# Kernel optimization log

Measured on AMD Instinct MI355X. Metric: run time of the kernel, lower is better.

## Reference

```python
import jax, jax.numpy as jnp
import numpy as np

B, T, D = 32, 1024, 768
H = 768          # GRU hidden size
INNER = 512      # fc output size
NOUT = 39        # out_proj outputs (13 classes x 3 ACCDOA coords)


def setup_inputs() -> dict:
    key = jax.random.key(0)
    ks = jax.random.split(key, 16)
    s_in = 1.0 / np.sqrt(H)
    inp = {
        "features": jax.random.normal(ks[0], (B, T, D), jnp.float32),
        "padding_mask": jnp.zeros((B, T), jnp.bool_),
        # GRU layer 0 (input D -> H), PyTorch gate order [r, z, n]
        "w_ih0": jax.random.uniform(ks[1], (3 * H, D), jnp.float32, -s_in, s_in),
        "w_hh0": jax.random.uniform(ks[2], (3 * H, H), jnp.float32, -s_in, s_in),
        "b_ih0": jax.random.uniform(ks[3], (3 * H,), jnp.float32, -s_in, s_in),
        "b_hh0": jax.random.uniform(ks[4], (3 * H,), jnp.float32, -s_in, s_in),
        # GRU layer 1 (H -> H)
        "w_ih1": jax.random.uniform(ks[5], (3 * H, H), jnp.float32, -s_in, s_in),
        "w_hh1": jax.random.uniform(ks[6], (3 * H, H), jnp.float32, -s_in, s_in),
        "b_ih1": jax.random.uniform(ks[7], (3 * H,), jnp.float32, -s_in, s_in),
        "b_hh1": jax.random.uniform(ks[8], (3 * H,), jnp.float32, -s_in, s_in),
        # fc: hidden -> inner, then SELU
        "fc_w": jax.random.uniform(ks[9], (INNER, H), jnp.float32, -s_in, s_in),
        "fc_b": jax.random.uniform(ks[10], (INNER,), jnp.float32, -s_in, s_in),
        # out_proj: inner -> num_outs, then tanh
        "out_w": jax.random.uniform(ks[11], (NOUT, INNER), jnp.float32, -1.0 / np.sqrt(INNER), 1.0 / np.sqrt(INNER)),
        "out_b": jax.random.uniform(ks[12], (NOUT,), jnp.float32, -1.0 / np.sqrt(INNER), 1.0 / np.sqrt(INNER)),
    }
    return inp


def _gru_layer(x, w_ih, w_hh, b_ih, b_hh):
    # x: [B, T, Din] -> [B, T, H]; PyTorch GRU math, gate order r,z,n
    b, t, _ = x.shape
    h = w_hh.shape[1]
    # precompute input projections for all timesteps in one big GEMM
    x_proj = jnp.einsum('btd,gd->btg', x, w_ih) + b_ih  # [B, T, 3H]

    def step(h_prev, xp):
        gi_r, gi_z, gi_n = jnp.split(xp, 3, axis=-1)
        gh = h_prev @ w_hh.T + b_hh
        gh_r, gh_z, gh_n = jnp.split(gh, 3, axis=-1)
        r = jax.nn.sigmoid(gi_r + gh_r)
        z = jax.nn.sigmoid(gi_z + gh_z)
        n = jnp.tanh(gi_n + r * gh_n)
        h_new = (1.0 - z) * n + z * h_prev
        return h_new, h_new

    h0 = jnp.zeros((b, h), x.dtype)
    _, ys = jax.lax.scan(step, h0, jnp.swapaxes(x_proj, 0, 1))  # ys: [T, B, H]
    return jnp.swapaxes(ys, 0, 1)


def reference(features, padding_mask, w_ih0, w_hh0, b_ih0, b_hh0,
              w_ih1, w_hh1, b_ih1, b_hh1, fc_w, fc_b, out_w, out_b):
    # dropout_input p=0.0 -> identity (eval); padding_mask unused by forward math
    x = _gru_layer(features, w_ih0, w_hh0, b_ih0, b_hh0)
    x = _gru_layer(x, w_ih1, w_hh1, b_ih1, b_hh1)
    x = jax.nn.selu(x @ fc_w.T + fc_b)          # fc + activation_fn='selu'
    x = jnp.tanh(x @ out_w.T + out_b)           # out_proj + out_activation 'tanh'
    return x
```

## Files before the change

### kernel.cpp

```cpp
#include <hip/hip_runtime.h>
#include <cstdint>

typedef float vf2 __attribute__((ext_vector_type(2)));

#define GB_M 128
#define GB_N 64
#define GB_K 16

__global__ __launch_bounds__(256) void gemm_bt_f32(
    const float* __restrict__ A, const float* __restrict__ B,
    const float* __restrict__ bias, float* __restrict__ C,
    int Mc, int N, int K, int tc_shift, int Tfull, int t0, int act)
{
  __shared__ float As[GB_K][GB_M + 4];
  __shared__ float Bs[GB_K][GB_N + 4];
  const int tid = threadIdx.x;
  const int m0 = blockIdx.y * GB_M;
  const int n0 = blockIdx.x * GB_N;
  const int tx = tid & 15;
  const int ty = tid >> 4;

  const int tcmask = (1 << tc_shift) - 1;
  int arow[2];
#pragma unroll
  for (int i = 0; i < 2; i++) {
    int f = tid + i * 256;
    int row = f >> 2;
    int rc = m0 + row;
    arow[i] = (rc >> tc_shift) * Tfull + t0 + (rc & tcmask);
  }
  const int akq = tid & 3;
  const int brow = tid >> 2;
  const int bn = n0 + brow;

  vf2 acc2[4][4];
#pragma unroll
  for (int i = 0; i < 4; i++)
#pragma unroll
    for (int j = 0; j < 4; j++) acc2[i][j] = (vf2)(0.f);

  for (int k0 = 0; k0 < K; k0 += GB_K) {
#pragma unroll
    for (int i = 0; i < 2; i++) {
      int f = tid + i * 256;
      int row = f >> 2;
      float4 v = *(const float4*)(A + (size_t)arow[i] * K + k0 + akq * 4);
      As[akq * 4 + 0][row] = v.x; As[akq * 4 + 1][row] = v.y;
      As[akq * 4 + 2][row] = v.z; As[akq * 4 + 3][row] = v.w;
    }
    {
      float4 v = make_float4(0.f, 0.f, 0.f, 0.f);
      if (bn < N) v = *(const float4*)(B + (size_t)bn * K + k0 + akq * 4);
      Bs[akq * 4 + 0][brow] = v.x; Bs[akq * 4 + 1][brow] = v.y;
      Bs[akq * 4 + 2][brow] = v.z; Bs[akq * 4 + 3][brow] = v.w;
    }
    __syncthreads();
#pragma unroll
    for (int k = 0; k < GB_K; k++) {
      float4 a0 = *(const float4*)&As[k][ty * 8];
      float4 a1 = *(const float4*)&As[k][ty * 8 + 4];
      float4 b0 = *(const float4*)&Bs[k][tx * 4];
      vf2 a2[4];
      a2[0] = (vf2){a0.x, a0.y}; a2[1] = (vf2){a0.z, a0.w};
      a2[2] = (vf2){a1.x, a1.y}; a2[3] = (vf2){a1.z, a1.w};
      float bv[4] = {b0.x, b0.y, b0.z, b0.w};
#pragma unroll
      for (int j = 0; j < 4; j++) {
        vf2 bs = (vf2){bv[j], bv[j]};
#pragma unroll
        for (int ip = 0; ip < 4; ip++)
          acc2[ip][j] = __builtin_elementwise_fma(a2[ip], bs, acc2[ip][j]);
      }
    }
    __syncthreads();
  }

#pragma unroll
  for (int j = 0; j < 4; j++) {
    int n = n0 + tx * 4 + j;
    if (n >= N) continue;
    float bz = bias[n];
#pragma unroll
    for (int i = 0; i < 8; i++) {
      int m = m0 + ty * 8 + i;
      float x = ((i & 1) ? acc2[i >> 1][j].y : acc2[i >> 1][j].x) + bz;
      if (act == 1) {
        x = 1.0507009873554805f * (x > 0.f ? x : 1.6732632423543772f * (__expf(x) - 1.f));
      } else if (act == 2) {
        x = tanhf(x);
      }
      C[(size_t)m * N + n] = x;
    }
  }
}

#define RT 384
#define RNWG 256

__global__ __launch_bounds__(RT, 1) void gru_rec(
    const float* __restrict__ gi, const float* __restrict__ w_hh,
    const float* __restrict__ b_hh, unsigned long long* __restrict__ gx,
    float* __restrict__ seq, int t0, int Tc)
{
  __shared__ float hs[8][776];
  const int wg = blockIdx.x;
  const int jg = wg & 63;
  const int sd = wg >> 6;
  const int j0 = jg * 12;
  const int tid = threadIdx.x;
  const int p  = tid >> 6;
  const int ks = tid & 63;

  float4 wreg[3][2][3];
#pragma unroll
  for (int g = 0; g < 3; g++)
#pragma unroll
    for (int j2 = 0; j2 < 2; j2++)
#pragma unroll
      for (int kk = 0; kk < 3; kk++)
        wreg[g][j2][kk] = *(const float4*)(
            w_hh + (size_t)(g * 768 + j0 + 2 * p + j2) * 768 + (kk * 64 + ks) * 4);

  const int j2l = (ks >> 2) & 1;
  const int cl  = ks & 3;
  const int j_out  = j0 + 2 * p + j2l;
  const int bX_out = 8 * sd + cl;
  const int bY_out = 8 * sd + 4 + cl;
  const float bhr = b_hh[j_out];
  const float bhz = b_hh[768 + j_out];
  const float bhn = b_hh[1536 + j_out];

  const int sbi = tid >> 6;
  const int sk  = tid & 63;

  const bool hi4 = (ks & 4) != 0;
  const bool hi2 = (ks & 2) != 0;
  const bool hi1 = (ks & 1) != 0;

  for (int tt = 0; tt < Tc; tt++) {
    const int t = t0 + tt;
    const unsigned wantt = (unsigned)t;

    float gXr = 0.f, gXz = 0.f, gXn = 0.f;
    if (ks < 8) {
      const float* gX = gi + ((size_t)bX_out * Tc + tt) * 2304 + j_out;
      gXr = gX[0]; gXz = gX[768]; gXn = gX[1536];
    }
    if (tid < 256) {
      const unsigned long long* src =
          gx + (size_t)(t & 1) * 24576 + (size_t)(8 * sd + sbi) * 768 + sk;
      unsigned long long v[12];
#pragma unroll
      for (int i = 0; i < 12; i++)
        v[i] = __hip_atomic_load(src + 64 * i, __ATOMIC_RELAXED, __HIP_MEMORY_SCOPE_AGENT);
      while (true) {
        unsigned miss = 0;
#pragma unroll
        for (int i = 0; i < 12; i++)
          miss |= (unsigned)((unsigned)(v[i] >> 32) < wantt);
        if (!miss) break;
        __builtin_amdgcn_s_sleep(1);
#pragma unroll
        for (int i = 0; i < 12; i++)
          if ((unsigned)(v[i] >> 32) < wantt)
            v[i] = __hip_atomic_load(src + 64 * i, __ATOMIC_RELAXED, __HIP_MEMORY_SCOPE_AGENT);
      }
#pragma unroll
      for (int i = 0; i < 12; i++)
        hs[sbi][sk + 64 * i] = __uint_as_float((unsigned)v[i]);
    }
    __syncthreads();

    float r3[3];
    {
      vf2 a2[3][2][4];
#pragma unroll
      for (int g = 0; g < 3; g++)
#pragma unroll
        for (int j2 = 0; j2 < 2; j2++)
#pragma unroll
          for (int c = 0; c < 4; c++) a2[g][j2][c] = (vf2)(0.f);
#pragma unroll
      for (int kk = 0; kk < 3; kk++) {
        const int off = (kk * 64 + ks) * 4;
        vf2 hlo[4], hhi[4];
#pragma unroll
        for (int c = 0; c < 4; c++) {
          float4 h = *(const float4*)(&hs[c][0] + off);
          hlo[c] = (vf2){h.x, h.y};
          hhi[c] = (vf2){h.z, h.w};
        }
#pragma unroll
        for (int g = 0; g < 3; g++)
#pragma unroll
          for (int j2 = 0; j2 < 2; j2++) {
            float4 w = wreg[g][j2][kk];
            vf2 wlo = (vf2){w.x, w.y};
            vf2 whi = (vf2){w.z, w.w};
#pragma unroll
            for (int c = 0; c < 4; c++) {
              a2[g][j2][c] = __builtin_elementwise_fma(wlo, hlo[c], a2[g][j2][c]);
              a2[g][j2][c] = __builtin_elementwise_fma(whi, hhi[c], a2[g][j2][c]);
            }
          }
      }
      float acc[3][2][4];
#pragma unroll
      for (int g = 0; g < 3; g++)
#pragma unroll
        for (int j2 = 0; j2 < 2; j2++)
#pragma unroll
          for (int c = 0; c < 4; c++) acc[g][j2][c] = a2[g][j2][c].x + a2[g][j2][c].y;

      float r12[3][4];
#pragma unroll
      for (int g = 0; g < 3; g++)
#pragma unroll
        for (int c = 0; c < 4; c++) {
          float send = hi4 ? acc[g][0][c] : acc[g][1][c];
          float keep = hi4 ? acc[g][1][c] : acc[g][0][c];
          r12[g][c] = keep + __shfl_xor(send, 4);
        }
      float r6[3][2];
#pragma unroll
      for (int g = 0; g < 3; g++)
#pragma unroll
        for (int c2 = 0; c2 < 2; c2++) {
          float send = hi2 ? r12[g][c2] : r12[g][2 + c2];
          float keep = hi2 ? r12[g][2 + c2] : r12[g][c2];
          r6[g][c2] = keep + __shfl_xor(send, 2);
        }
#pragma unroll
      for (int g = 0; g < 3; g++) {
        float send = hi1 ? r6[g][0] : r6[g][1];
        float keep = hi1 ? r6[g][1] : r6[g][0];
        r3[g] = keep + __shfl_xor(send, 1);
      }
#pragma unroll
      for (int g = 0; g < 3; g++) {
        r3[g] += __shfl_xor(r3[g], 8);
        r3[g] += __shfl_xor(r3[g], 16);
        r3[g] += __shfl_xor(r3[g], 32);
      }
    }
    if (ks < 8) {
      float hp = hs[cl][j_out];
      float r = 1.f / (1.f + __expf(-(gXr + r3[0] + bhr)));
      float z = 1.f / (1.f + __expf(-(gXz + r3[1] + bhz)));
      float n = tanhf(gXn + r * (r3[2] + bhn));
      float hv = (1.f - z) * n + z * hp;
      __hip_atomic_store(
          gx + (size_t)((t + 1) & 1) * 24576 + (size_t)bX_out * 768 + j_out,
          ((unsigned long long)(unsigned)(t + 1) << 32) |
              (unsigned long long)__float_as_uint(hv),
          __ATOMIC_RELAXED, __HIP_MEMORY_SCOPE_AGENT);
      seq[((size_t)bX_out * 1024 + t) * 768 + j_out] = hv;
    }

    float gYr = 0.f, gYz = 0.f, gYn = 0.f;
    if (ks < 8) {
      const float* gY = gi + ((size_t)bY_out * Tc + tt) * 2304 + j_out;
      gYr = gY[0]; gYz = gY[768]; gYn = gY[1536];
    }
    if (tid < 256) {
      const unsigned long long* src =
          gx + (size_t)(t & 1) * 24576 + (size_t)(8 * sd + 4 + sbi) * 768 + sk;
      unsigned long long v[12];
#pragma unroll
      for (int i = 0; i < 12; i++)
        v[i] = __hip_atomic_load(src + 64 * i, __ATOMIC_RELAXED, __HIP_MEMORY_SCOPE_AGENT);
      while (true) {
        unsigned miss = 0;
#pragma unroll
        for (int i = 0; i < 12; i++)
          miss |= (unsigned)((unsigned)(v[i] >> 32) < wantt);
        if (!miss) break;
        __builtin_amdgcn_s_sleep(1);
#pragma unroll
        for (int i = 0; i < 12; i++)
          if ((unsigned)(v[i] >> 32) < wantt)
            v[i] = __hip_atomic_load(src + 64 * i, __ATOMIC_RELAXED, __HIP_MEMORY_SCOPE_AGENT);
      }
#pragma unroll
      for (int i = 0; i < 12; i++)
        hs[4 + sbi][sk + 64 * i] = __uint_as_float((unsigned)v[i]);
    }
    __syncthreads();

    {
      vf2 a2[3][2][4];
#pragma unroll
      for (int g = 0; g < 3; g++)
#pragma unroll
        for (int j2 = 0; j2 < 2; j2++)
#pragma unroll
          for (int c = 0; c < 4; c++) a2[g][j2][c] = (vf2)(0.f);
#pragma unroll
      for (int kk = 0; kk < 3; kk++) {
        const int off = (kk * 64 + ks) * 4;
        vf2 hlo[4], hhi[4];
#pragma unroll
        for (int c = 0; c < 4; c++) {
          float4 h = *(const float4*)(&hs[4 + c][0] + off);
          hlo[c] = (vf2){h.x, h.y};
          hhi[c] = (vf2){h.z, h.w};
        }
#pragma unroll
        for (int g = 0; g < 3; g++)
#pragma unroll
          for (int j2 = 0; j2 < 2; j2++) {
            float4 w = wreg[g][j2][kk];
            vf2 wlo = (vf2){w.x, w.y};
            vf2 whi = (vf2){w.z, w.w};
#pragma unroll
            for (int c = 0; c < 4; c++) {
              a2[g][j2][c] = __builtin_elementwise_fma(wlo, hlo[c], a2[g][j2][c]);
              a2[g][j2][c] = __builtin_elementwise_fma(whi, hhi[c], a2[g][j2][c]);
            }
          }
      }
      float acc[3][2][4];
#pragma unroll
      for (int g = 0; g < 3; g++)
#pragma unroll
        for (int j2 = 0; j2 < 2; j2++)
#pragma unroll
          for (int c = 0; c < 4; c++) acc[g][j2][c] = a2[g][j2][c].x + a2[g][j2][c].y;

      float r12[3][4];
#pragma unroll
      for (int g = 0; g < 3; g++)
#pragma unroll
        for (int c = 0; c < 4; c++) {
          float send = hi4 ? acc[g][0][c] : acc[g][1][c];
          float keep = hi4 ? acc[g][1][c] : acc[g][0][c];
          r12[g][c] = keep + __shfl_xor(send, 4);
        }
      float r6[3][2];
#pragma unroll
      for (int g = 0; g < 3; g++)
#pragma unroll
        for (int c2 = 0; c2 < 2; c2++) {
          float send = hi2 ? r12[g][c2] : r12[g][2 + c2];
          float keep = hi2 ? r12[g][2 + c2] : r12[g][c2];
          r6[g][c2] = keep + __shfl_xor(send, 2);
        }
#pragma unroll
      for (int g = 0; g < 3; g++) {
        float send = hi1 ? r6[g][0] : r6[g][1];
        float keep = hi1 ? r6[g][1] : r6[g][0];
        r3[g] = keep + __shfl_xor(send, 1);
      }
#pragma unroll
      for (int g = 0; g < 3; g++) {
        r3[g] += __shfl_xor(r3[g], 8);
        r3[g] += __shfl_xor(r3[g], 16);
        r3[g] += __shfl_xor(r3[g], 32);
      }
    }
    if (ks < 8) {
      float hp = hs[4 + cl][j_out];
      float r = 1.f / (1.f + __expf(-(gYr + r3[0] + bhr)));
      float z = 1.f / (1.f + __expf(-(gYz + r3[1] + bhz)));
      float n = tanhf(gYn + r * (r3[2] + bhn));
      float hv = (1.f - z) * n + z * hp;
      __hip_atomic_store(
          gx + (size_t)((t + 1) & 1) * 24576 + (size_t)bY_out * 768 + j_out,
          ((unsigned long long)(unsigned)(t + 1) << 32) |
              (unsigned long long)__float_as_uint(hv),
          __ATOMIC_RELAXED, __HIP_MEMORY_SCOPE_AGENT);
      seq[((size_t)bY_out * 1024 + t) * 768 + j_out] = hv;
    }
  }
}

extern "C" void kernel_launch(void* const* d_in, const int* in_sizes, int n_in,
                              void* d_out, int out_size, void* d_ws, size_t ws_size,
                              hipStream_t stream) {
  const float* feat  = (const float*)d_in[0];
  const float* w_ih0 = (const float*)d_in[2];
  const float* w_hh0 = (const float*)d_in[3];
  const float* b_ih0 = (const float*)d_in[4];
  const float* b_hh0 = (const float*)d_in[5];
  const float* w_ih1 = (const float*)d_in[6];
  const float* w_hh1 = (const float*)d_in[7];
  const float* b_ih1 = (const float*)d_in[8];
  const float* b_hh1 = (const float*)d_in[9];
  const float* fc_w  = (const float*)d_in[10];
  const float* fc_b  = (const float*)d_in[11];
  const float* out_w = (const float*)d_in[12];
  const float* out_b = (const float*)d_in[13];
  float* out = (float*)d_out;

  const int Tc = 256;
  const int McChunk = 32 * Tc;

  float* proj = (float*)d_ws;
  float* seq  = proj + (size_t)32 * Tc * 2304;
  unsigned long long* gx = (unsigned long long*)(seq + (size_t)25165824);
  const size_t GXB = (size_t)2 * 24576 * 8;

  hipMemsetAsync(gx, 0, GXB, stream);
  for (int c = 0; c < 4; c++) {
    gemm_bt_f32<<<dim3(36, McChunk / 128), dim3(256), 0, stream>>>(
        feat, w_ih0, b_ih0, proj, McChunk, 2304, 768, 8, 1024, c * Tc, 0);
    gru_rec<<<dim3(RNWG), dim3(RT), 0, stream>>>(
        proj, w_hh0, b_hh0, gx, seq, c * Tc, Tc);
  }
  hipMemsetAsync(gx, 0, GXB, stream);
  for (int c = 0; c < 4; c++) {
    gemm_bt_f32<<<dim3(36, McChunk / 128), dim3(256), 0, stream>>>(
        seq, w_ih1, b_ih1, proj, McChunk, 2304, 768, 8, 1024, c * Tc, 0);
    gru_rec<<<dim3(RNWG), dim3(RT), 0, stream>>>(
        proj, w_hh1, b_hh1, gx, seq, c * Tc, Tc);
  }
  gemm_bt_f32<<<dim3(8, 256), dim3(256), 0, stream>>>(
      seq, fc_w, fc_b, proj, 32768, 512, 768, 15, 32768, 0, 1);
  gemm_bt_f32<<<dim3(1, 256), dim3(256), 0, stream>>>(
      proj, out_w, out_b, out, 32768, 39, 512, 15, 32768, 0, 2);
}
```

Before: 12.29 ms.

## Fuse both GRU layers into one wavefront-skewed persistent recurrence kernel

Runs layer 0 step r and layer 1 step r-1 in the same persistent kernel, so the two recurrences share each round's synchronisation instead of running as two separate sequential scans. Layer 1's input projection is computed inside the loop from a slice of w_ih1 kept in LDS, which removes the layer-1 input GEMM launches and the full layer-0 sequence write and re-read. Each step does more work per round (three dot products instead of one), with more register and LDS pressure and a dual-flag spin wait. The hs layout loses its row padding, which may add LDS bank conflicts.

Result: slower. 32.44 ms (+163.9%).

```diff
diff --git a/kernel.cpp b/kernel.cpp
--- a/kernel.cpp
+++ b/kernel.cpp
@@ -97,12 +97,17 @@
 #define RT 384
 #define RNWG 256
 
-__global__ __launch_bounds__(RT, 1) void gru_rec(
-    const float* __restrict__ gi, const float* __restrict__ w_hh,
-    const float* __restrict__ b_hh, unsigned long long* __restrict__ gx,
-    float* __restrict__ seq, int t0, int Tc)
+__global__ __launch_bounds__(RT, 1) void gru_rec_dual(
+    const float* __restrict__ gi0,
+    const float* __restrict__ w_hh0, const float* __restrict__ b_hh0,
+    const float* __restrict__ w_hh1, const float* __restrict__ b_hh1,
+    const float* __restrict__ w_ih1, const float* __restrict__ b_ih1,
+    unsigned long long* __restrict__ gx0, unsigned long long* __restrict__ gx1,
+    float* __restrict__ seq1, int t0, int Tc, int rounds)
 {
-  __shared__ float hs[8][776];
+  __shared__ float hs0[8][768];
+  __shared__ float hs1[8][768];
+  __shared__ float wih[36][768];
   const int wg = blockIdx.x;
   const int jg = wg & 63;
   const int sd = wg >> 6;
@@ -111,24 +116,30 @@
   const int p  = tid >> 6;
   const int ks = tid & 63;
 
-  float4 wreg[3][2][3];
+  float4 wreg0[3][2][3], wreg1[3][2][3];
 #pragma unroll
   for (int g = 0; g < 3; g++)
 #pragma unroll
     for (int j2 = 0; j2 < 2; j2++)
 #pragma unroll
-      for (int kk = 0; kk < 3; kk++)
-        wreg[g][j2][kk] = *(const float4*)(
-            w_hh + (size_t)(g * 768 + j0 + 2 * p + j2) * 768 + (kk * 64 + ks) * 4);
+      for (int kk = 0; kk < 3; kk++) {
+        const size_t row = (size_t)(g * 768 + j0 + 2 * p + j2) * 768 + (kk * 64 + ks) * 4;
+        wreg0[g][j2][kk] = *(const float4*)(w_hh0 + row);
+        wreg1[g][j2][kk] = *(const float4*)(w_hh1 + row);
+        *(float4*)&wih[(g * 2 + j2) * 6 + p][(kk * 64 + ks) * 4] =
+            *(const float4*)(w_ih1 + row);
+      }
 
   const int j2l = (ks >> 2) & 1;
   const int cl  = ks & 3;
-  const int j_out  = j0 + 2 * p + j2l;
-  const int bX_out = 8 * sd + cl;
-  const int bY_out = 8 * sd + 4 + cl;
-  const float bhr = b_hh[j_out];
-  const float bhz = b_hh[768 + j_out];
-  const float bhn = b_hh[1536 + j_out];
+  const int j_out = j0 + 2 * p + j2l;
+  const float bh0r = b_hh0[j_out];
+  const float bh0z = b_hh0[768 + j_out];
+  const float bh0n = b_hh0[1536 + j_out];
+  const float c1r  = b_ih1[j_out] + b_hh1[j_out];
+  const float c1z  = b_ih1[768 + j_out] + b_hh1[768 + j_out];
+  const float bi1n = b_ih1[1536 + j_out];
+  const float bh1n = b_hh1[1536 + j_out];
 
   const int sbi = tid >> 6;
   const int sk  = tid & 63;
@@ -137,239 +148,217 @@
   const bool hi2 = (ks & 2) != 0;
   const bool hi1 = (ks & 1) != 0;
 
-  for (int tt = 0; tt < Tc; tt++) {
-    const int t = t0 + tt;
-    const unsigned wantt = (unsigned)t;
-
-    float gXr = 0.f, gXz = 0.f, gXn = 0.f;
-    if (ks < 8) {
-      const float* gX = gi + ((size_t)bX_out * Tc + tt) * 2304 + j_out;
-      gXr = gX[0]; gXz = gX[768]; gXn = gX[1536];
-    }
-    if (tid < 256) {
-      const unsigned long long* src =
-          gx + (size_t)(t & 1) * 24576 + (size_t)(8 * sd + sbi) * 768 + sk;
-      unsigned long long v[12];
-#pragma unroll
-      for (int i = 0; i < 12; i++)
-        v[i] = __hip_atomic_load(src + 64 * i, __ATOMIC_RELAXED, __HIP_MEMORY_SCOPE_AGENT);
-      while (true) {
-        unsigned miss = 0;
+  auto ladder = [&](vf2 (&a2)[3][2][4], float* r3) {
+    float acc[3][2][4];
+#pragma unroll
+    for (int g = 0; g < 3; g++)
+#pragma unroll
+      for (int j2 = 0; j2 < 2; j2++)
+#pragma unroll
+        for (int c = 0; c < 4; c++) acc[g][j2][c] = a2[g][j2][c].x + a2[g][j2][c].y;
+    float r12[3][4];
+#pragma unroll
+    for (int g = 0; g < 3; g++)
+#pragma unroll
+      for (int c = 0; c < 4; c++) {
+        float send = hi4 ? acc[g][0][c] : acc[g][1][c];
+        float keep = hi4 ? acc[g][1][c] : acc[g][0][c];
+        r12[g][c] = keep + __shfl_xor(send, 4);
+      }
+    float r6[3][2];
+#pragma unroll
+    for (int g = 0; g < 3; g++)
+#pragma unroll
+      for (int c2 = 0; c2 < 2; c2++) {
+        float send = hi2 ? r12[g][c2] : r12[g][2 + c2];
+        float keep = hi2 ? r12[g][2 + c2] : r12[g][c2];
+        r6[g][c2] = keep + __shfl_xor(send, 2);
+      }
+#pragma unroll
+    for (int g = 0; g < 3; g++) {
+      float send = hi1 ? r6[g][0] : r6[g][1];
+      float keep = hi1 ? r6[g][1] : r6[g][0];
+      r3[g] = keep + __shfl_xor(send, 1);
+    }
+#pragma unroll
+    for (int g = 0; g < 3; g++) {
+      r3[g] += __shfl_xor(r3[g], 8);
+      r3[g] += __shfl_xor(r3[g], 16);
+      r3[g] += __shfl_xor(r3[g], 32);
+    }
+  };
+
+  auto dotreg = [&](const float4 (&wr)[3][2][3], const float (*h)[768], float* r3) {
+    vf2 a2[3][2][4];
+#pragma unroll
+    for (int g = 0; g < 3; g++)
+#pragma unroll
+      for (int j2 = 0; j2 < 2; j2++)
+#pragma unroll
+        for (int c = 0; c < 4; c++) a2[g][j2][c] = (vf2)(0.f);
+#pragma unroll
+    for (int kk = 0; kk < 3; kk++) {
+      const int off = (kk * 64 + ks) * 4;
+      vf2 hlo[4], hhi[4];
+#pragma unroll
+      for (int c = 0; c < 4; c++) {
+        float4 x = *(const float4*)(h[c] + off);
+        hlo[c] = (vf2){x.x, x.y};
+        hhi[c] = (vf2){x.z, x.w};
+      }
+#pragma unroll
+      for (int g = 0; g < 3; g++)
+#pragma unroll
+        for (int j2 = 0; j2 < 2; j2++) {
+          float4 w = wr[g][j2][kk];
+          vf2 wlo = (vf2){w.x, w.y};
+          vf2 whi = (vf2){w.z, w.w};
+#pragma unroll
+          for (int c = 0; c < 4; c++) {
+            a2[g][j2][c] = __builtin_elementwise_fma(wlo, hlo[c], a2[g][j2][c]);
+            a2[g][j2][c] = __builtin_elementwise_fma(whi, hhi[c], a2[g][j2][c]);
+          }
+        }
+    }
+    ladder(a2, r3);
+  };
+
+  auto dotlds = [&](const float (*h)[768], float* r3) {
+    vf2 a2[3][2][4];
+#pragma unroll
+    for (int g = 0; g < 3; g++)
+#pragma unroll
+      for (int j2 = 0; j2 < 2; j2++)
+#pragma unroll
+        for (int c = 0; c < 4; c++) a2[g][j2][c] = (vf2)(0.f);
+#pragma unroll
+    for (int kk = 0; kk < 3; kk++) {
+      const int off = (kk * 64 + ks) * 4;
+      vf2 hlo[4], hhi[4];
+#pragma unroll
+      for (int c = 0; c < 4; c++) {
+        float4 x = *(const float4*)(h[c] + off);
+        hlo[c] = (vf2){x.x, x.y};
+        hhi[c] = (vf2){x.z, x.w};
+      }
+#pragma unroll
+      for (int g = 0; g < 3; g++)
+#pragma unroll
+        for (int j2 = 0; j2 < 2; j2++) {
+          float4 w = *(const float4*)&wih[(g * 2 + j2) * 6 + p][off];
+          vf2 wlo = (vf2){w.x, w.y};
+          vf2 whi = (vf2){w.z, w.w};
+#pragma unroll
+          for (int c = 0; c < 4; c++) {
+            a2[g][j2][c] = __builtin_elementwise_fma(wlo, hlo[c], a2[g][j2][c]);
+            a2[g][j2][c] = __builtin_elementwise_fma(whi, hhi[c], a2[g][j2][c]);
+          }
+        }
+    }
+    ladder(a2, r3);
+  };
+
+  __syncthreads();
+
+  for (int rr = 0; rr < rounds; rr++) {
+    const int r = t0 + rr;
+    const int s = r - 1;
+    const bool doL0 = (r < 1024);
+    const bool doL1 = (s >= 0);
+
+#pragma unroll 1
+    for (int half = 0; half < 2; half++) {
+      const int hb = 4 * half;
+
+      float g0r = 0.f, g0z = 0.f, g0n = 0.f;
+      if (doL0 && ks < 8) {
+        const float* gp = gi0 + ((size_t)(8 * sd + hb + cl) * Tc + rr) * 2304 + j_out;
+        g0r = gp[0]; g0z = gp[768]; g0n = gp[1536];
+      }
+
+      if (tid < 256) {
+        const unsigned long long* s0p =
+            gx0 + (size_t)(r & 1) * 24576 + (size_t)(8 * sd + hb + sbi) * 768 + sk;
+        unsigned long long v0[12];
 #pragma unroll
         for (int i = 0; i < 12; i++)
-          miss |= (unsigned)((unsigned)(v[i] >> 32) < wantt);
-        if (!miss) break;
-        __builtin_amdgcn_s_sleep(1);
+          v0[i] = __hip_atomic_load(s0p + 64 * i, __ATOMIC_RELAXED, __HIP_MEMORY_SCOPE_AGENT);
+        const unsigned long long* s1p = nullptr;
+        unsigned long long v1[12];
+        if (doL1) {
+          s1p = gx1 + (size_t)(s & 1) * 24576 + (size_t)(8 * sd + hb + sbi) * 768 + sk;
+#pragma unroll
+          for (int i = 0; i < 12; i++)
+            v1[i] = __hip_atomic_load(s1p + 64 * i, __ATOMIC_RELAXED, __HIP_MEMORY_SCOPE_AGENT);
+        }
+        const unsigned w0 = (unsigned)r, w1 = (unsigned)s;
+        while (true) {
+          unsigned miss = 0;
+#pragma unroll
+          for (int i = 0; i < 12; i++)
+            miss |= (unsigned)((unsigned)(v0[i] >> 32) < w0);
+          if (doL1)
+#pragma unroll
+            for (int i = 0; i < 12; i++)
+              miss |= (unsigned)((unsigned)(v1[i] >> 32) < w1);
+          if (!miss) break;
+          __builtin_amdgcn_s_sleep(1);
+#pragma unroll
+          for (int i = 0; i < 12; i++)
+            if ((unsigned)(v0[i] >> 32) < w0)
+              v0[i] = __hip_atomic_load(s0p + 64 * i, __ATOMIC_RELAXED, __HIP_MEMORY_SCOPE_AGENT);
+          if (doL1)
+#pragma unroll
+            for (int i = 0; i < 12; i++)
+              if ((unsigned)(v1[i] >> 32) < w1)
+                v1[i] = __hip_atomic_load(s1p + 64 * i, __ATOMIC_RELAXED, __HIP_MEMORY_SCOPE_AGENT);
+        }
 #pragma unroll
         for (int i = 0; i < 12; i++)
-          if ((unsigned)(v[i] >> 32) < wantt)
-            v[i] = __hip_atomic_load(src + 64 * i, __ATOMIC_RELAXED, __HIP_MEMORY_SCOPE_AGENT);
-      }
-#pragma unroll
-      for (int i = 0; i < 12; i++)
-        hs[sbi][sk + 64 * i] = __uint_as_float((unsigned)v[i]);
-    }
-    __syncthreads();
-
-    float r3[3];
-    {
-      vf2 a2[3][2][4];
-#pragma unroll
-      for (int g = 0; g < 3; g++)
-#pragma unroll
-        for (int j2 = 0; j2 < 2; j2++)
-#pragma unroll
-          for (int c = 0; c < 4; c++) a2[g][j2][c] = (vf2)(0.f);
-#pragma unroll
-      for (int kk = 0; kk < 3; kk++) {
-        const int off = (kk * 64 + ks) * 4;
-        vf2 hlo[4], hhi[4];
-#pragma unroll
-        for (int c = 0; c < 4; c++) {
-          float4 h = *(const float4*)(&hs[c][0] + off);
-          hlo[c] = (vf2){h.x, h.y};
-          hhi[c] = (vf2){h.z, h.w};
-        }
-#pragma unroll
-        for (int g = 0; g < 3; g++)
-#pragma unroll
-          for (int j2 = 0; j2 < 2; j2++) {
-            float4 w = wreg[g][j2][kk];
-            vf2 wlo = (vf2){w.x, w.y};
-            vf2 whi = (vf2){w.z, w.w};
-#pragma unroll
-            for (int c = 0; c < 4; c++) {
-              a2[g][j2][c] = __builtin_elementwise_fma(wlo, hlo[c], a2[g][j2][c]);
-              a2[g][j2][c] = __builtin_elementwise_fma(whi, hhi[c], a2[g][j2][c]);
-            }
-          }
-      }
-      float acc[3][2][4];
-#pragma unroll
-      for (int g = 0; g < 3; g++)
-#pragma unroll
-        for (int j2 = 0; j2 < 2; j2++)
-#pragma unroll
-          for (int c = 0; c < 4; c++) acc[g][j2][c] = a2[g][j2][c].x + a2[g][j2][c].y;
-
-      float r12[3][4];
-#pragma unroll
-      for (int g = 0; g < 3; g++)
-#pragma unroll
-        for (int c = 0; c < 4; c++) {
-          float send = hi4 ? acc[g][0][c] : acc[g][1][c];
-          float keep = hi4 ? acc[g][1][c] : acc[g][0][c];
-          r12[g][c] = keep + __shfl_xor(send, 4);
-        }
-      float r6[3][2];
-#pragma unroll
-      for (int g = 0; g < 3; g++)
-#pragma unroll
-        for (int c2 = 0; c2 < 2; c2++) {
-          float send = hi2 ? r12[g][c2] : r12[g][2 + c2];
-          float keep = hi2 ? r12[g][2 + c2] : r12[g][c2];
-          r6[g][c2] = keep + __shfl_xor(send, 2);
-        }
-#pragma unroll
-      for (int g = 0; g < 3; g++) {
-        float send = hi1 ? r6[g][0] : r6[g][1];
-        float keep = hi1 ? r6[g][1] : r6[g][0];
-        r3[g] = keep + __shfl_xor(send, 1);
-      }
-#pragma unroll
-      for (int g = 0; g < 3; g++) {
-        r3[g] += __shfl_xor(r3[g], 8);
-        r3[g] += __shfl_xor(r3[g], 16);
-        r3[g] += __shfl_xor(r3[g], 32);
-      }
-    }
-    if (ks < 8) {
-      float hp = hs[cl][j_out];
-      float r = 1.f / (1.f + __expf(-(gXr + r3[0] + bhr)));
-      float z = 1.f / (1.f + __expf(-(gXz + r3[1] + bhz)));
-      float n = tanhf(gXn + r * (r3[2] + bhn));
-      float hv = (1.f - z) * n + z * hp;
-      __hip_atomic_store(
-          gx + (size_t)((t + 1) & 1) * 24576 + (size_t)bX_out * 768 + j_out,
-          ((unsigned long long)(unsigned)(t + 1) << 32) |
-              (unsigned long long)__float_as_uint(hv),
-          __ATOMIC_RELAXED, __HIP_MEMORY_SCOPE_AGENT);
-      seq[((size_t)bX_out * 1024 + t) * 768 + j_out] = hv;
-    }
-
-    float gYr = 0.f, gYz = 0.f, gYn = 0.f;
-    if (ks < 8) {
-      const float* gY = gi + ((size_t)bY_out * Tc + tt) * 2304 + j_out;
-      gYr = gY[0]; gYz = gY[768]; gYn = gY[1536];
-    }
-    if (tid < 256) {
-      const unsigned long long* src =
-          gx + (size_t)(t & 1) * 24576 + (size_t)(8 * sd + 4 + sbi) * 768 + sk;
-      unsigned long long v[12];
-#pragma unroll
-      for (int i = 0; i < 12; i++)
-        v[i] = __hip_atomic_load(src + 64 * i, __ATOMIC_RELAXED, __HIP_MEMORY_SCOPE_AGENT);
-      while (true) {
-        unsigned miss = 0;
-#pragma unroll
-        for (int i = 0; i < 12; i++)
-          miss |= (unsigned)((unsigned)(v[i] >> 32) < wantt);
-        if (!miss) break;
-        __builtin_amdgcn_s_sleep(1);
-#pragma unroll
-        for (int i = 0; i < 12; i++)
-          if ((unsigned)(v[i] >> 32) < wantt)
-            v[i] = __hip_atomic_load(src + 64 * i, __ATOMIC_RELAXED, __HIP_MEMORY_SCOPE_AGENT);
-      }
-#pragma unroll
-      for (int i = 0; i < 12; i++)
-        hs[4 + sbi][sk + 64 * i] = __uint_as_float((unsigned)v[i]);
-    }
-    __syncthreads();
-
-    {
-      vf2 a2[3][2][4];
-#pragma unroll
-      for (int g = 0; g < 3; g++)
-#pragma unroll
-        for (int j2 = 0; j2 < 2; j2++)
-#pragma unroll
-          for (int c = 0; c < 4; c++) a2[g][j2][c] = (vf2)(0.f);
-#pragma unroll
-      for (int kk = 0; kk < 3; kk++) {
-        const int off = (kk * 64 + ks) * 4;
-        vf2 hlo[4], hhi[4];
-#pragma unroll
-        for (int c = 0; c < 4; c++) {
-          float4 h = *(const float4*)(&hs[4 + c][0] + off);
-          hlo[c] = (vf2){h.x, h.y};
-          hhi[c] = (vf2){h.z, h.w};
-        }
-#pragma unroll
-        for (int g = 0; g < 3; g++)
-#pragma unroll
-          for (int j2 = 0; j2 < 2; j2++) {
-            float4 w = wreg[g][j2][kk];
-            vf2 wlo = (vf2){w.x, w.y};
-            vf2 whi = (vf2){w.z, w.w};
-#pragma unroll
-            for (int c = 0; c < 4; c++) {
-              a2[g][j2][c] = __builtin_elementwise_fma(wlo, hlo[c], a2[g][j2][c]);
-              a2[g][j2][c] = __builtin_elementwise_fma(whi, hhi[c], a2[g][j2][c]);
-            }
-          }
-      }
-      float acc[3][2][4];
-#pragma unroll
-      for (int g = 0; g < 3; g++)
-#pragma unroll
-        for (int j2 = 0; j2 < 2; j2++)
-#pragma unroll
-          for (int c = 0; c < 4; c++) acc[g][j2][c] = a2[g][j2][c].x + a2[g][j2][c].y;
-
-      float r12[3][4];
-#pragma unroll
-      for (int g = 0; g < 3; g++)
-#pragma unroll
-        for (int c = 0; c < 4; c++) {
-          float send = hi4 ? acc[g][0][c] : acc[g][1][c];
-          float keep = hi4 ? acc[g][1][c] : acc[g][0][c];
-          r12[g][c] = keep + __shfl_xor(send, 4);
-        }
-      float r6[3][2];
-#pragma unroll
-      for (int g = 0; g < 3; g++)
-#pragma unroll
-        for (int c2 = 0; c2 < 2; c2++) {
-          float send = hi2 ? r12[g][c2] : r12[g][2 + c2];
-          float keep = hi2 ? r12[g][2 + c2] : r12[g][c2];
-          r6[g][c2] = keep + __shfl_xor(send, 2);
-        }
-#pragma unroll
-      for (int g = 0; g < 3; g++) {
-        float send = hi1 ? r6[g][0] : r6[g][1];
-        float keep = hi1 ? r6[g][1] : r6[g][0];
-        r3[g] = keep + __shfl_xor(send, 1);
-      }
-#pragma unroll
-      for (int g = 0; g < 3; g++) {
-        r3[g] += __shfl_xor(r3[g], 8);
-        r3[g] += __shfl_xor(r3[g], 16);
-        r3[g] += __shfl_xor(r3[g], 32);
-      }
-    }
-    if (ks < 8) {
-      float hp = hs[4 + cl][j_out];
-      float r = 1.f / (1.f + __expf(-(gYr + r3[0] + bhr)));
-      float z = 1.f / (1.f + __expf(-(gYz + r3[1] + bhz)));
-      float n = tanhf(gYn + r * (r3[2] + bhn));
-      float hv = (1.f - z) * n + z * hp;
-      __hip_atomic_store(
-          gx + (size_t)((t + 1) & 1) * 24576 + (size_t)bY_out * 768 + j_out,
-          ((unsigned long long)(unsigned)(t + 1) << 32) |
-              (unsigned long long)__float_as_uint(hv),
-          __ATOMIC_RELAXED, __HIP_MEMORY_SCOPE_AGENT);
-      seq[((size_t)bY_out * 1024 + t) * 768 + j_out] = hv;
+          hs0[hb + sbi][sk + 64 * i] = __uint_as_float((unsigned)v0[i]);
+        if (doL1)
+#pragma unroll
+          for (int i = 0; i < 12; i++)
+            hs1[hb + sbi][sk + 64 * i] = __uint_as_float((unsigned)v1[i]);
+      }
+      __syncthreads();
+
+      if (doL0) {
+        float r3[3];
+        dotreg(wreg0, &hs0[hb], r3);
+        if (ks < 8) {
+          float hp = hs0[hb + cl][j_out];
+          float rg = 1.f / (1.f + __expf(-(g0r + r3[0] + bh0r)));
+          float zg = 1.f / (1.f + __expf(-(g0z + r3[1] + bh0z)));
+          float ng = tanhf(g0n + rg * (r3[2] + bh0n));
+          float hv = (1.f - zg) * ng + zg * hp;
+          __hip_atomic_store(
+              gx0 + (size_t)((r + 1) & 1) * 24576 + (size_t)(8 * sd + hb + cl) * 768 + j_out,
+              ((unsigned long long)(unsigned)(r + 1) << 32) |
+                  (unsigned long long)__float_as_uint(hv),
+              __ATOMIC_RELAXED, __HIP_MEMORY_SCOPE_AGENT);
+        }
+      }
+
+      if (doL1) {
+        float rhh[3], rih[3];
+        dotreg(wreg1, &hs1[hb], rhh);
+        dotlds(&hs0[hb], rih);
+        if (ks < 8) {
+          float hp = hs1[hb + cl][j_out];
+          float rg = 1.f / (1.f + __expf(-(rih[0] + rhh[0] + c1r)));
+          float zg = 1.f / (1.f + __expf(-(rih[1] + rhh[1] + c1z)));
+          float ng = tanhf(rih[2] + bi1n + rg * (rhh[2] + bh1n));
+          float hv = (1.f - zg) * ng + zg * hp;
+          __hip_atomic_store(
+              gx1 + (size_t)((s + 1) & 1) * 24576 + (size_t)(8 * sd + hb + cl) * 768 + j_out,
+              ((unsigned long long)(unsigned)(s + 1) << 32) |
+                  (unsigned long long)__float_as_uint(hv),
+              __ATOMIC_RELAXED, __HIP_MEMORY_SCOPE_AGENT);
+          seq1[((size_t)(8 * sd + hb + cl) * 1024 + s) * 768 + j_out] = hv;
+        }
+      }
+      __syncthreads();
     }
   }
 }
@@ -396,26 +385,21 @@
   const int McChunk = 32 * Tc;
 
   float* proj = (float*)d_ws;
-  float* seq  = proj + (size_t)32 * Tc * 2304;
-  unsigned long long* gx = (unsigned long long*)(seq + (size_t)25165824);
-  const size_t GXB = (size_t)2 * 24576 * 8;
-
-  hipMemsetAsync(gx, 0, GXB, stream);
+  float* seq1 = proj + (size_t)18874368;
+  unsigned long long* gx0 = (unsigned long long*)(seq1 + (size_t)25165824);
+  unsigned long long* gx1 = gx0 + 49152;
+
+  hipMemsetAsync(gx0, 0, 2 * 393216, stream);
+
   for (int c = 0; c < 4; c++) {
     gemm_bt_f32<<<dim3(36, McChunk / 128), dim3(256), 0, stream>>>(
         feat, w_ih0, b_ih0, proj, McChunk, 2304, 768, 8, 1024, c * Tc, 0);
-    gru_rec<<<dim3(RNWG), dim3(RT), 0, stream>>>(
-        proj, w_hh0, b_hh0, gx, seq, c * Tc, Tc);
-  }
-  hipMemsetAsync(gx, 0, GXB, stream);
-  for (int c = 0; c < 4; c++) {
-    gemm_bt_f32<<<dim3(36, McChunk / 128), dim3(256), 0, stream>>>(
-        seq, w_ih1, b_ih1, proj, McChunk, 2304, 768, 8, 1024, c * Tc, 0);
-    gru_rec<<<dim3(RNWG), dim3(RT), 0, stream>>>(
-        proj, w_hh1, b_hh1, gx, seq, c * Tc, Tc);
+    gru_rec_dual<<<dim3(RNWG), dim3(RT), 0, stream>>>(
+        proj, w_hh0, b_hh0, w_hh1, b_hh1, w_ih1, b_ih1,
+        gx0, gx1, seq1, c * Tc, Tc, (c == 3) ? Tc + 1 : Tc);
   }
   gemm_bt_f32<<<dim3(8, 256), dim3(256), 0, stream>>>(
-      seq, fc_w, fc_b, proj, 32768, 512, 768, 15, 32768, 0, 1);
+      seq1, fc_w, fc_b, proj, 32768, 512, 768, 15, 32768, 0, 1);
   gemm_bt_f32<<<dim3(1, 256), dim3(256), 0, stream>>>(
       proj, out_w, out_b, out, 32768, 39, 512, 15, 32768, 0, 2);
 }
```
